# Kernel tuning notes

Hardware: AMD Instinct MI355X
Metric: run time of the kernel (lower is better)

Reference implementation:

```python
import jax, jax.numpy as jnp
import numpy as np

B, C, N, K, OUT = 4, 128, 8192, 20, 128


def setup_inputs() -> dict:
    key = jax.random.key(0)
    k1, k2, k3 = jax.random.split(key, 3)
    x = jax.random.normal(k1, (B, C, N), dtype=jnp.float32)
    W = jax.random.normal(k2, (OUT, 2 * C), dtype=jnp.float32) * 0.02  # 1x1 conv weight over 2C edge channels
    b = jnp.zeros((OUT,), dtype=jnp.float32)
    return {"x": x, "W": W, "b": b}


def _knn_idx(x, k):
    # x: [B, C, N]; pairwise_distance = -||xi - xj||^2 (larger = closer)
    inner = -2.0 * jnp.einsum('bcn,bcm->bnm', x, x)          # [B,N,N]
    xx = jnp.sum(x * x, axis=1)                               # [B,N]
    pd = -xx[:, :, None] - inner - xx[:, None, :]             # [B,N,N]
    return jax.lax.top_k(pd, k)[1]                            # [B,N,k] int32


def reference(x, W, b):
    k = K
    idx = _knn_idx(x, k)                                      # [B,N,k]
    xt = jnp.transpose(x, (0, 2, 1))                          # [B,N,C]
    nbr = jax.vmap(lambda xb, ib: xb[ib])(xt, idx)            # [B,N,k,C] gather
    center = jnp.broadcast_to(xt[:, :, None, :], nbr.shape)   # [B,N,k,C]
    # torch: cat((x, x - feature), dim=3)
    edge = jnp.concatenate([center, center - nbr], axis=-1)   # [B,N,k,2C]
    # 1x1 Conv2d over channel dim + ReLU
    h = jnp.einsum('bnkc,oc->bonk', edge, W) + b[None, :, None, None]
    h = jax.nn.relu(h)
    # aggregate over neighbors (EdgeConv max pooling)
    return jnp.max(h, axis=-1)                                # [B,OUT,N]
```

## Files before the change

### kernel.cpp

```cpp
#include <hip/hip_runtime.h>
#include <float.h>

#define Bz   4
#define Cz   128
#define Nz   8192
#define Kz   20
#define OUTz 128

__global__ __launch_bounds__(256) void xx_kernel(const float* __restrict__ x,
                                                 float* __restrict__ xx) {
    int t = blockIdx.x * 256 + threadIdx.x;
    int b = t >> 13;
    int n = t & (Nz - 1);
    const float* xp = x + (size_t)b * Cz * Nz + n;
    float s = 0.f;
#pragma unroll 8
    for (int c = 0; c < Cz; ++c) {
        float v = xp[(size_t)c * Nz];
        s = fmaf(v, v, s);
    }
    xx[t] = s;
}

__global__ __launch_bounds__(256) void knn_kernel(const float* __restrict__ x,
                                                  const float* __restrict__ xxg,
                                                  int* __restrict__ idxout) {
    const int b  = blockIdx.y;
    const int q0 = blockIdx.x * 64;

    __shared__ __align__(16) float Ald[128 * 64];
    __shared__ __align__(16) float buf2[2 * 8 * 256];
    float* bufA = buf2;
    float* bufB = buf2 + 2048;
    float* sc   = buf2;

    const int tid  = threadIdx.x;
    const int tx   = tid & 31;
    const int ty   = tid >> 5;
    const int lane = tid & 63;
    const int wid  = tid >> 6;

    const float* xb = x + (size_t)b * Cz * Nz;

    {
        int q4 = (tid & 15) * 4;
        int c0 = tid >> 4;
#pragma unroll
        for (int rep = 0; rep < 8; ++rep) {
            int c = c0 + rep * 16;
            *(float4*)&Ald[c * 64 + q4] =
                *(const float4*)&xb[(size_t)c * Nz + q0 + q4];
        }
    }

    float tv[Kz];
    int   ti[Kz];
#pragma unroll
    for (int s = 0; s < Kz; ++s) { tv[s] = -FLT_MAX; ti[s] = 0; }
    float wv = -FLT_MAX;
    int wslot = 0;
    const int orow = wid * 16 + lane;
    const int srow = wid * 16 + (lane & 15);
    const int part = lane >> 4;

    float4 st0[2], st1[2];

#define LOADCHUNK(dst, kj, ch)                                                \
    {                                                                         \
        _Pragma("unroll")                                                     \
        for (int i = 0; i < 2; ++i)                                           \
            dst[i] = *(const float4*)&xb[(size_t)((ch) * 8 + ty) * Nz + (kj) + tx * 4 + i * 128]; \
    }

#define WRITECHUNK(src, buf)                                                  \
    {                                                                         \
        _Pragma("unroll")                                                     \
        for (int i = 0; i < 2; ++i)                                           \
            *(float4*)&(buf)[ty * 256 + tx * 4 + i * 128] = src[i];           \
    }

#define COMPUTECHUNK(buf, ch)                                                 \
    {                                                                         \
        _Pragma("unroll")                                                     \
        for (int cc = 0; cc < 8; ++cc) {                                      \
            float4 a0 = *(const float4*)&Ald[((ch) * 8 + cc) * 64 + ty * 8];  \
            float4 a1 = *(const float4*)&Ald[((ch) * 8 + cc) * 64 + ty * 8 + 4]; \
            float4 b0 = *(const float4*)&(buf)[cc * 256 + tx * 4];            \
            float4 b1 = *(const float4*)&(buf)[cc * 256 + 128 + tx * 4];      \
            float av[8] = {a0.x, a0.y, a0.z, a0.w, a1.x, a1.y, a1.z, a1.w};   \
            float bv[8] = {b0.x, b0.y, b0.z, b0.w, b1.x, b1.y, b1.z, b1.w};   \
            _Pragma("unroll")                                                 \
            for (int q = 0; q < 8; ++q) {                                     \
                _Pragma("unroll")                                             \
                for (int k = 0; k < 8; ++k)                                   \
                    acc[q][k] = fmaf(av[q], bv[k], acc[q][k]);                \
            }                                                                 \
        }                                                                     \
    }

#define EXTRACT(pm_, gbase_)                                                  \
    {                                                                         \
        unsigned long long pm = (pm_);                                        \
        while (pm) {                                                          \
            int j = __ffsll(pm) - 1;                                          \
            pm &= pm - 1;                                                     \
            float s = sc[orow * 64 + ((j + 4 * orow) & 63)];                  \
            if (s > wv) {                                                     \
                int gj = (gbase_) + j;                                        \
                _Pragma("unroll")                                             \
                for (int s2 = 0; s2 < Kz; ++s2) {                             \
                    bool hit = (s2 == wslot);                                 \
                    tv[s2] = hit ? s : tv[s2];                                \
                    ti[s2] = hit ? gj : ti[s2];                               \
                }                                                             \
                wv = tv[0]; wslot = 0;                                        \
                _Pragma("unroll")                                             \
                for (int s2 = 1; s2 < Kz; ++s2)                               \
                    if (tv[s2] < wv) { wv = tv[s2]; wslot = s2; }             \
            }                                                                 \
        }                                                                     \
    }

    LOADCHUNK(st0, 0, 0);

#pragma unroll 1
    for (int kt = 0; kt < Nz / 256; ++kt) {
        const int kj0 = kt * 256;
        const int kjn = ((kt + 1) & (Nz / 256 - 1)) * 256;

        float acc[8][8];
#pragma unroll
        for (int q = 0; q < 8; ++q)
#pragma unroll
            for (int k = 0; k < 8; ++k) acc[q][k] = 0.f;

#pragma unroll 1
        for (int cp = 0; cp < 8; ++cp) {
            const int e = 2 * cp;
            WRITECHUNK(st0, bufA);
            __syncthreads();
            LOADCHUNK(st1, kj0, e + 1);
            COMPUTECHUNK(bufA, e);
            WRITECHUNK(st1, bufB);
            __syncthreads();
            if (e == 14) { LOADCHUNK(st0, kjn, 0); }
            else         { LOADCHUNK(st0, kj0, e + 2); }
            COMPUTECHUNK(bufB, e + 1);
        }
        __syncthreads();

        float4 xxlo = *(const float4*)&xxg[b * Nz + kj0 + tx * 4];
        float4 xxhi = *(const float4*)&xxg[b * Nz + kj0 + 128 + tx * 4];
        float xxa[8] = {xxlo.x, xxlo.y, xxlo.z, xxlo.w,
                        xxhi.x, xxhi.y, xxhi.z, xxhi.w};
        const int txh = tx >> 4;
        const int cl0 = (tx & 15) * 4;

#pragma unroll
        for (int h = 0; h < 4; ++h) {
            if (txh == (h & 1)) {
                const int qs = (h >> 1) * 4;
#pragma unroll
                for (int dq = 0; dq < 8; ++dq) {
                    int r = ty * 8 + dq;
                    float4 w;
                    w.x = 2.f * acc[dq][qs + 0] - xxa[qs + 0];
                    w.y = 2.f * acc[dq][qs + 1] - xxa[qs + 1];
                    w.z = 2.f * acc[dq][qs + 2] - xxa[qs + 2];
                    w.w = 2.f * acc[dq][qs + 3] - xxa[qs + 3];
                    *(float4*)&sc[r * 64 + ((cl0 + 4 * r) & 63)] = w;
                }
            }
            __syncthreads();

            float wvb = __shfl(wv, lane & 15);
            unsigned m = 0;
#pragma unroll
            for (int g = 0; g < 4; ++g) {
                int col = part * 16 + g * 4;
                float4 v = *(const float4*)&sc[srow * 64 + ((col + 4 * srow) & 63)];
                m |= (unsigned)(v.x > wvb) << (4 * g + 0);
                m |= (unsigned)(v.y > wvb) << (4 * g + 1);
                m |= (unsigned)(v.z > wvb) << (4 * g + 2);
                m |= (unsigned)(v.w > wvb) << (4 * g + 3);
            }
            unsigned long long f = (unsigned long long)m << (16 * part);
            f |= __shfl_xor(f, 16);
            f |= __shfl_xor(f, 32);
            if (lane < 16) { EXTRACT(f, kj0 + h * 64); }
            __syncthreads();
        }
    }

    if (lane < 16) {
        size_t base = ((size_t)b * Nz + q0 + orow) * Kz;
#pragma unroll
        for (int s = 0; s < Kz; ++s) idxout[base + s] = ti[s];
    }
#undef LOADCHUNK
#undef WRITECHUNK
#undef COMPUTECHUNK
#undef EXTRACT
}

__global__ __launch_bounds__(256) void feat_kernel(const float* __restrict__ x,
                                                   const float* __restrict__ W,
                                                   const float* __restrict__ bias,
                                                   float* __restrict__ Y) {
    const int gp0 = blockIdx.x * 64;
    const int b   = gp0 >> 13;
    const int n0  = gp0 & (Nz - 1);
    const int o0  = blockIdx.y * 64;

    __shared__ __align__(16) float xt[128 * 64];
    __shared__ __align__(16) float wt[128 * 64];

    const int tid = threadIdx.x;
    const int tx  = tid & 15;
    const int ty  = tid >> 4;

    {
        int li = tid & 63;
        int c0 = tid >> 6;
        const float* xbp = x + (size_t)b * Cz * Nz + n0;
#pragma unroll
        for (int rep = 0; rep < 32; ++rep) {
            int c = c0 + rep * 4;
            xt[c * 64 + li] = xbp[(size_t)c * Nz + li];
        }
    }
    {
        int lo = tid & 63;
        int c0 = tid >> 6;
        int oo = o0 + lo;
#pragma unroll
        for (int rep = 0; rep < 32; ++rep) {
            int c = c0 + rep * 4;
            float w;
            if (oo < 128) w = W[oo * 256 + c] + W[oo * 256 + 128 + c];
            else          w = W[(oo - 128) * 256 + 128 + c];
            wt[c * 64 + lo] = w;
        }
    }
    __syncthreads();

    float acc[4][4];
#pragma unroll
    for (int di = 0; di < 4; ++di)
#pragma unroll
        for (int dj = 0; dj < 4; ++dj) acc[di][dj] = 0.f;

    const int aoff = ty * 4;
    const int boff = tx * 4;
#pragma unroll 8
    for (int c = 0; c < 128; ++c) {
        float4 a  = *(const float4*)&xt[c * 64 + aoff];
        float4 ww = *(const float4*)&wt[c * 64 + boff];
        float av[4] = {a.x, a.y, a.z, a.w};
        float wvv[4] = {ww.x, ww.y, ww.z, ww.w};
#pragma unroll
        for (int di = 0; di < 4; ++di)
#pragma unroll
            for (int dj = 0; dj < 4; ++dj)
                acc[di][dj] = fmaf(av[di], wvv[dj], acc[di][dj]);
    }

    float4 bv = make_float4(0.f, 0.f, 0.f, 0.f);
    if (o0 < 128) bv = *(const float4*)&bias[o0 + tx * 4];
#pragma unroll
    for (int di = 0; di < 4; ++di) {
        float4 r;
        r.x = acc[di][0] + bv.x;
        r.y = acc[di][1] + bv.y;
        r.z = acc[di][2] + bv.z;
        r.w = acc[di][3] + bv.w;
        *(float4*)&Y[(size_t)(gp0 + ty * 4 + di) * 256 + o0 + tx * 4] = r;
    }
}

__global__ __launch_bounds__(256) void gather_kernel(const int* __restrict__ idxg,
                                                     const float* __restrict__ Y,
                                                     float* __restrict__ out) {
    const int gp0 = blockIdx.x * 64;
    const int b   = gp0 >> 13;
    const int n0  = gp0 & (Nz - 1);

    __shared__ int lidx[64 * 21];
    const int tid = threadIdx.x;
    for (int t = tid; t < 64 * Kz; t += 256) {
        int p = t / Kz, j = t - p * Kz;
        lidx[p * 21 + j] = idxg[(size_t)(gp0 + p) * Kz + j];
    }
    __syncthreads();

    const int p  = tid & 63;
    const int o0 = (tid >> 6) * 32;

    float mn[32];
#pragma unroll
    for (int q = 0; q < 32; ++q) mn[q] = FLT_MAX;

    for (int j = 0; j < Kz; ++j) {
        int m = lidx[p * 21 + j];
        const float4* vr =
            (const float4*)(Y + (size_t)(b * Nz + m) * 256 + 128 + o0);
#pragma unroll
        for (int q = 0; q < 8; ++q) {
            float4 v4 = vr[q];
            mn[4 * q + 0] = fminf(mn[4 * q + 0], v4.x);
            mn[4 * q + 1] = fminf(mn[4 * q + 1], v4.y);
            mn[4 * q + 2] = fminf(mn[4 * q + 2], v4.z);
            mn[4 * q + 3] = fminf(mn[4 * q + 3], v4.w);
        }
    }

    const float4* ur = (const float4*)(Y + (size_t)(gp0 + p) * 256 + o0);
#pragma unroll
    for (int q = 0; q < 8; ++q) {
        float4 u4 = ur[q];
        float r0 = fmaxf(u4.x - mn[4 * q + 0], 0.f);
        float r1 = fmaxf(u4.y - mn[4 * q + 1], 0.f);
        float r2 = fmaxf(u4.z - mn[4 * q + 2], 0.f);
        float r3 = fmaxf(u4.w - mn[4 * q + 3], 0.f);
        size_t ob = ((size_t)b * OUTz + o0 + 4 * q) * Nz + n0 + p;
        out[ob + 0 * Nz] = r0;
        out[ob + 1 * Nz] = r1;
        out[ob + 2 * Nz] = r2;
        out[ob + 3 * Nz] = r3;
    }
}

extern "C" void kernel_launch(void* const* d_in, const int* in_sizes, int n_in,
                              void* d_out, int out_size, void* d_ws, size_t ws_size,
                              hipStream_t stream) {
    const float* x    = (const float*)d_in[0];
    const float* W    = (const float*)d_in[1];
    const float* bias = (const float*)d_in[2];
    float* out = (float*)d_out;

    char* ws = (char*)d_ws;
    float* xx  = (float*)ws;
    int*   idx = (int*)(ws + (1 << 17));
    float* Y   = (float*)(ws + (4 << 20));

    xx_kernel<<<dim3(Bz * Nz / 256), dim3(256), 0, stream>>>(x, xx);

    knn_kernel<<<dim3(Nz / 64, Bz), dim3(256), 0, stream>>>(x, xx, idx);

    feat_kernel<<<dim3(Bz * Nz / 64, 4), dim3(256), 0, stream>>>(x, W, bias, Y);

    gather_kernel<<<dim3(Bz * Nz / 64), dim3(256), 0, stream>>>(idx, Y, out);
}
```

Baseline: 1.296 ms.

## Split KNN candidate range across two blocks and merge partial top-k lists

The KNN kernel now processes only half of the candidate points per block, using a third grid dimension, and writes partial top-k values and indices to workspace. A new merge kernel combines the two partial lists per query into the final indices. This doubles the number of blocks to improve GPU occupancy and load balance, at the cost of extra workspace traffic, a second kernel launch, and a fresh threshold per half that triggers more insertions.

```diff
diff --git a/kernel.cpp b/kernel.cpp
--- a/kernel.cpp
+++ b/kernel.cpp
@@ -24,9 +24,12 @@
 
 __global__ __launch_bounds__(256) void knn_kernel(const float* __restrict__ x,
                                                   const float* __restrict__ xxg,
-                                                  int* __restrict__ idxout) {
+                                                  float* __restrict__ pval,
+                                                  int* __restrict__ pidx) {
     const int b  = blockIdx.y;
     const int q0 = blockIdx.x * 64;
+    const int hz = blockIdx.z;
+    const int kb = hz * (Nz / 2);
 
     __shared__ __align__(16) float Ald[128 * 64];
     __shared__ __align__(16) float buf2[2 * 8 * 256];
@@ -121,12 +124,12 @@
         }                                                                     \
     }
 
-    LOADCHUNK(st0, 0, 0);
+    LOADCHUNK(st0, kb, 0);
 
 #pragma unroll 1
-    for (int kt = 0; kt < Nz / 256; ++kt) {
-        const int kj0 = kt * 256;
-        const int kjn = ((kt + 1) & (Nz / 256 - 1)) * 256;
+    for (int kt = 0; kt < Nz / 2 / 256; ++kt) {
+        const int kj0 = kb + kt * 256;
+        const int kjn = kb + (((kt + 1) & (Nz / 2 / 256 - 1)) * 256);
 
         float acc[8][8];
 #pragma unroll
@@ -193,14 +196,56 @@
     }
 
     if (lane < 16) {
-        size_t base = ((size_t)b * Nz + q0 + orow) * Kz;
-#pragma unroll
-        for (int s = 0; s < Kz; ++s) idxout[base + s] = ti[s];
+        size_t base = ((size_t)hz * Bz * Nz + (size_t)b * Nz + q0 + orow) * Kz;
+#pragma unroll
+        for (int s = 0; s < Kz; ++s) { pval[base + s] = tv[s]; pidx[base + s] = ti[s]; }
     }
 #undef LOADCHUNK
 #undef WRITECHUNK
 #undef COMPUTECHUNK
 #undef EXTRACT
+}
+
+__global__ __launch_bounds__(256) void merge_kernel(const float* __restrict__ pval,
+                                                    const int* __restrict__ pidx,
+                                                    int* __restrict__ idxout) {
+    const int r = blockIdx.x * 256 + threadIdx.x;
+    const float* v0 = pval + (size_t)r * Kz;
+    const float* v1 = pval + ((size_t)Bz * Nz + r) * Kz;
+    const int*   i0 = pidx + (size_t)r * Kz;
+    const int*   i1 = pidx + ((size_t)Bz * Nz + r) * Kz;
+
+    float tv[Kz]; int ti[Kz];
+#pragma unroll
+    for (int s = 0; s < Kz; ++s) { tv[s] = v0[s]; ti[s] = i0[s]; }
+    float wv = tv[0]; int wi = ti[0]; int wslot = 0;
+#pragma unroll
+    for (int s = 1; s < Kz; ++s) {
+        bool worse = (tv[s] < wv) || (tv[s] == wv && ti[s] > wi);
+        if (worse) { wv = tv[s]; wi = ti[s]; wslot = s; }
+    }
+#pragma unroll 1
+    for (int c = 0; c < Kz; ++c) {
+        float cv = v1[c]; int ci = i1[c];
+        bool better = (cv > wv) || (cv == wv && ci < wi);
+        if (better) {
+#pragma unroll
+            for (int s = 0; s < Kz; ++s) {
+                bool hit = (s == wslot);
+                tv[s] = hit ? cv : tv[s];
+                ti[s] = hit ? ci : ti[s];
+            }
+            wv = tv[0]; wi = ti[0]; wslot = 0;
+#pragma unroll
+            for (int s = 1; s < Kz; ++s) {
+                bool worse = (tv[s] < wv) || (tv[s] == wv && ti[s] > wi);
+                if (worse) { wv = tv[s]; wi = ti[s]; wslot = s; }
+            }
+        }
+    }
+    size_t base = (size_t)r * Kz;
+#pragma unroll
+    for (int s = 0; s < Kz; ++s) idxout[base + s] = ti[s];
 }
 
 __global__ __launch_bounds__(256) void feat_kernel(const float* __restrict__ x,
@@ -339,13 +384,17 @@
     float* out = (float*)d_out;
 
     char* ws = (char*)d_ws;
-    float* xx  = (float*)ws;
-    int*   idx = (int*)(ws + (1 << 17));
-    float* Y   = (float*)(ws + (4 << 20));
+    float* xx   = (float*)ws;
+    int*   idx  = (int*)(ws + (1 << 17));
+    float* pval = (float*)(ws + (4 << 20));
+    int*   pidx = (int*)(ws + (10 << 20));
+    float* Y    = (float*)(ws + (4 << 20));
 
     xx_kernel<<<dim3(Bz * Nz / 256), dim3(256), 0, stream>>>(x, xx);
 
-    knn_kernel<<<dim3(Nz / 64, Bz), dim3(256), 0, stream>>>(x, xx, idx);
+    knn_kernel<<<dim3(Nz / 64, Bz, 2), dim3(256), 0, stream>>>(x, xx, pval, pidx);
+
+    merge_kernel<<<dim3(Bz * Nz / 256), dim3(256), 0, stream>>>(pval, pidx, idx);
 
     feat_kernel<<<dim3(Bz * Nz / 64, 4), dim3(256), 0, stream>>>(x, W, bias, Y);
 
```

Result: slower. 1.412 ms (+8.9%).

## Stream kNN key tile from global memory into registers, drop LDS staging

Applied to the files above, without the earlier changes.

The kNN distance GEMM stops staging key columns through double-buffered shared memory with barriers. Each thread now loads its float4 of key columns straight from global memory into registers, prefetching four channels ahead, and reads the query tile from LDS as broadcast. The register tile changes from 8x8 to 16x4 per thread, which removes the per-chunk __syncthreads and LDS writes. In exchange, each key element is loaded by all four waves instead of once per block, which raises global/L2 traffic, and each FMA now needs more LDS reads.

```diff
diff --git a/kernel.cpp b/kernel.cpp
--- a/kernel.cpp
+++ b/kernel.cpp
@@ -29,14 +29,9 @@
     const int q0 = blockIdx.x * 64;
 
     __shared__ __align__(16) float Ald[128 * 64];
-    __shared__ __align__(16) float buf2[2 * 8 * 256];
-    float* bufA = buf2;
-    float* bufB = buf2 + 2048;
-    float* sc   = buf2;
+    __shared__ __align__(16) float sc[64 * 64];
 
     const int tid  = threadIdx.x;
-    const int tx   = tid & 31;
-    const int ty   = tid >> 5;
     const int lane = tid & 63;
     const int wid  = tid >> 6;
 
@@ -52,6 +47,7 @@
                 *(const float4*)&xb[(size_t)c * Nz + q0 + q4];
         }
     }
+    __syncthreads();
 
     float tv[Kz];
     int   ti[Kz];
@@ -62,39 +58,27 @@
     const int orow = wid * 16 + lane;
     const int srow = wid * 16 + (lane & 15);
     const int part = lane >> 4;
-
-    float4 st0[2], st1[2];
-
-#define LOADCHUNK(dst, kj, ch)                                                \
+    const int aoff = wid * 16;
+
+#define CSTEP(vb, cc)                                                         \
     {                                                                         \
+        const float4 cur_ = vb;                                               \
+        vb = *(const float4*)&bp[(size_t)(((cc) + 4) & 127) * Nz];            \
+        const float* ar_ = &Ald[(cc) * 64 + aoff];                            \
+        float4 a0_ = *(const float4*)(ar_);                                   \
+        float4 a1_ = *(const float4*)(ar_ + 4);                               \
+        float4 a2_ = *(const float4*)(ar_ + 8);                               \
+        float4 a3_ = *(const float4*)(ar_ + 12);                              \
+        float av_[16] = {a0_.x, a0_.y, a0_.z, a0_.w,                          \
+                         a1_.x, a1_.y, a1_.z, a1_.w,                          \
+                         a2_.x, a2_.y, a2_.z, a2_.w,                          \
+                         a3_.x, a3_.y, a3_.z, a3_.w};                         \
         _Pragma("unroll")                                                     \
-        for (int i = 0; i < 2; ++i)                                           \
-            dst[i] = *(const float4*)&xb[(size_t)((ch) * 8 + ty) * Nz + (kj) + tx * 4 + i * 128]; \
-    }
-
-#define WRITECHUNK(src, buf)                                                  \
-    {                                                                         \
-        _Pragma("unroll")                                                     \
-        for (int i = 0; i < 2; ++i)                                           \
-            *(float4*)&(buf)[ty * 256 + tx * 4 + i * 128] = src[i];           \
-    }
-
-#define COMPUTECHUNK(buf, ch)                                                 \
-    {                                                                         \
-        _Pragma("unroll")                                                     \
-        for (int cc = 0; cc < 8; ++cc) {                                      \
-            float4 a0 = *(const float4*)&Ald[((ch) * 8 + cc) * 64 + ty * 8];  \
-            float4 a1 = *(const float4*)&Ald[((ch) * 8 + cc) * 64 + ty * 8 + 4]; \
-            float4 b0 = *(const float4*)&(buf)[cc * 256 + tx * 4];            \
-            float4 b1 = *(const float4*)&(buf)[cc * 256 + 128 + tx * 4];      \
-            float av[8] = {a0.x, a0.y, a0.z, a0.w, a1.x, a1.y, a1.z, a1.w};   \
-            float bv[8] = {b0.x, b0.y, b0.z, b0.w, b1.x, b1.y, b1.z, b1.w};   \
-            _Pragma("unroll")                                                 \
-            for (int q = 0; q < 8; ++q) {                                     \
-                _Pragma("unroll")                                             \
-                for (int k = 0; k < 8; ++k)                                   \
-                    acc[q][k] = fmaf(av[q], bv[k], acc[q][k]);                \
-            }                                                                 \
+        for (int q = 0; q < 16; ++q) {                                        \
+            acc[q][0] = fmaf(av_[q], cur_.x, acc[q][0]);                      \
+            acc[q][1] = fmaf(av_[q], cur_.y, acc[q][1]);                      \
+            acc[q][2] = fmaf(av_[q], cur_.z, acc[q][2]);                      \
+            acc[q][3] = fmaf(av_[q], cur_.w, acc[q][3]);                      \
         }                                                                     \
     }
 
@@ -121,54 +105,48 @@
         }                                                                     \
     }
 
-    LOADCHUNK(st0, 0, 0);
-
 #pragma unroll 1
-    for (int kt = 0; kt < Nz / 256; ++kt) {
-        const int kj0 = kt * 256;
-        const int kjn = ((kt + 1) & (Nz / 256 - 1)) * 256;
-
-        float acc[8][8];
-#pragma unroll
-        for (int q = 0; q < 8; ++q)
-#pragma unroll
-            for (int k = 0; k < 8; ++k) acc[q][k] = 0.f;
+    for (int kp = 0; kp < Nz / 256; ++kp) {
+        const float* bp = xb + kp * 256 + 4 * lane;
+
+        float acc[16][4];
+#pragma unroll
+        for (int q = 0; q < 16; ++q)
+#pragma unroll
+            for (int i = 0; i < 4; ++i) acc[q][i] = 0.f;
+
+        float4 vb0 = *(const float4*)&bp[0];
+        float4 vb1 = *(const float4*)&bp[(size_t)1 * Nz];
+        float4 vb2 = *(const float4*)&bp[(size_t)2 * Nz];
+        float4 vb3 = *(const float4*)&bp[(size_t)3 * Nz];
 
 #pragma unroll 1
-        for (int cp = 0; cp < 8; ++cp) {
-            const int e = 2 * cp;
-            WRITECHUNK(st0, bufA);
-            __syncthreads();
-            LOADCHUNK(st1, kj0, e + 1);
-            COMPUTECHUNK(bufA, e);
-            WRITECHUNK(st1, bufB);
-            __syncthreads();
-            if (e == 14) { LOADCHUNK(st0, kjn, 0); }
-            else         { LOADCHUNK(st0, kj0, e + 2); }
-            COMPUTECHUNK(bufB, e + 1);
-        }
-        __syncthreads();
-
-        float4 xxlo = *(const float4*)&xxg[b * Nz + kj0 + tx * 4];
-        float4 xxhi = *(const float4*)&xxg[b * Nz + kj0 + 128 + tx * 4];
-        float xxa[8] = {xxlo.x, xxlo.y, xxlo.z, xxlo.w,
-                        xxhi.x, xxhi.y, xxhi.z, xxhi.w};
-        const int txh = tx >> 4;
-        const int cl0 = (tx & 15) * 4;
-
+        for (int c4 = 0; c4 < 16; ++c4) {
+            const int c = 8 * c4;
+            CSTEP(vb0, c + 0)
+            CSTEP(vb1, c + 1)
+            CSTEP(vb2, c + 2)
+            CSTEP(vb3, c + 3)
+            CSTEP(vb0, c + 4)
+            CSTEP(vb1, c + 5)
+            CSTEP(vb2, c + 6)
+            CSTEP(vb3, c + 7)
+        }
+
+        const float4 xxk = *(const float4*)&xxg[b * Nz + kp * 256 + 4 * lane];
 #pragma unroll
         for (int h = 0; h < 4; ++h) {
-            if (txh == (h & 1)) {
-                const int qs = (h >> 1) * 4;
-#pragma unroll
-                for (int dq = 0; dq < 8; ++dq) {
-                    int r = ty * 8 + dq;
+            if ((lane >> 4) == h) {
+                const int cl = (lane & 15) * 4;
+#pragma unroll
+                for (int dq = 0; dq < 16; ++dq) {
+                    int r = wid * 16 + dq;
                     float4 w;
-                    w.x = 2.f * acc[dq][qs + 0] - xxa[qs + 0];
-                    w.y = 2.f * acc[dq][qs + 1] - xxa[qs + 1];
-                    w.z = 2.f * acc[dq][qs + 2] - xxa[qs + 2];
-                    w.w = 2.f * acc[dq][qs + 3] - xxa[qs + 3];
-                    *(float4*)&sc[r * 64 + ((cl0 + 4 * r) & 63)] = w;
+                    w.x = 2.f * acc[dq][0] - xxk.x;
+                    w.y = 2.f * acc[dq][1] - xxk.y;
+                    w.z = 2.f * acc[dq][2] - xxk.z;
+                    w.w = 2.f * acc[dq][3] - xxk.w;
+                    *(float4*)&sc[r * 64 + ((cl + 4 * r) & 63)] = w;
                 }
             }
             __syncthreads();
@@ -187,7 +165,7 @@
             unsigned long long f = (unsigned long long)m << (16 * part);
             f |= __shfl_xor(f, 16);
             f |= __shfl_xor(f, 32);
-            if (lane < 16) { EXTRACT(f, kj0 + h * 64); }
+            if (lane < 16) { EXTRACT(f, kp * 256 + h * 64); }
             __syncthreads();
         }
     }
@@ -197,9 +175,7 @@
 #pragma unroll
         for (int s = 0; s < Kz; ++s) idxout[base + s] = ti[s];
     }
-#undef LOADCHUNK
-#undef WRITECHUNK
-#undef COMPUTECHUNK
+#undef CSTEP
 #undef EXTRACT
 }
 
```

Result: slower. 2.260 ms (+74.4%).

## Load key tiles directly from global into registers, dropping LDS staging

Applied to the files above, without the earlier changes.

The kNN distance GEMM no longer stages the 256-wide key tile through double-buffered shared memory with block-wide barriers. Each thread instead streams its own key columns from global memory into a 4-deep register prefetch ring and consumes them directly. The aim is to remove LDS writes and __syncthreads from the inner channel loop, and to shrink shared memory to a dedicated score buffer. In exchange, each wavefront row (the 8 ty groups) loads the same key data redundantly from global/L2, and prefetch depth is limited, so memory latency may be exposed.

```diff
diff --git a/kernel.cpp b/kernel.cpp
--- a/kernel.cpp
+++ b/kernel.cpp
@@ -29,10 +29,7 @@
     const int q0 = blockIdx.x * 64;
 
     __shared__ __align__(16) float Ald[128 * 64];
-    __shared__ __align__(16) float buf2[2 * 8 * 256];
-    float* bufA = buf2;
-    float* bufB = buf2 + 2048;
-    float* sc   = buf2;
+    __shared__ __align__(16) float sc[64 * 64];
 
     const int tid  = threadIdx.x;
     const int tx   = tid & 31;
@@ -52,6 +49,7 @@
                 *(const float4*)&xb[(size_t)c * Nz + q0 + q4];
         }
     }
+    __syncthreads();
 
     float tv[Kz];
     int   ti[Kz];
@@ -63,38 +61,28 @@
     const int srow = wid * 16 + (lane & 15);
     const int part = lane >> 4;
 
-    float4 st0[2], st1[2];
-
-#define LOADCHUNK(dst, kj, ch)                                                \
+#define CSTEP(u, cc)                                                          \
     {                                                                         \
+        const float4 cur0_ = rb0[u];                                          \
+        const float4 cur1_ = rb1[u];                                          \
+        const int cn_ = ((cc) + 4) & 127;                                     \
+        rb0[u] = *(const float4*)&bp0[(size_t)cn_ * Nz];                      \
+        rb1[u] = *(const float4*)&bp1[(size_t)cn_ * Nz];                      \
+        const float* ar_ = &Ald[(cc) * 64 + ty * 8];                          \
+        float4 a0_ = *(const float4*)(ar_);                                   \
+        float4 a1_ = *(const float4*)(ar_ + 4);                               \
+        float av_[8] = {a0_.x, a0_.y, a0_.z, a0_.w,                           \
+                        a1_.x, a1_.y, a1_.z, a1_.w};                          \
         _Pragma("unroll")                                                     \
-        for (int i = 0; i < 2; ++i)                                           \
-            dst[i] = *(const float4*)&xb[(size_t)((ch) * 8 + ty) * Nz + (kj) + tx * 4 + i * 128]; \
-    }
-
-#define WRITECHUNK(src, buf)                                                  \
-    {                                                                         \
-        _Pragma("unroll")                                                     \
-        for (int i = 0; i < 2; ++i)                                           \
-            *(float4*)&(buf)[ty * 256 + tx * 4 + i * 128] = src[i];           \
-    }
-
-#define COMPUTECHUNK(buf, ch)                                                 \
-    {                                                                         \
-        _Pragma("unroll")                                                     \
-        for (int cc = 0; cc < 8; ++cc) {                                      \
-            float4 a0 = *(const float4*)&Ald[((ch) * 8 + cc) * 64 + ty * 8];  \
-            float4 a1 = *(const float4*)&Ald[((ch) * 8 + cc) * 64 + ty * 8 + 4]; \
-            float4 b0 = *(const float4*)&(buf)[cc * 256 + tx * 4];            \
-            float4 b1 = *(const float4*)&(buf)[cc * 256 + 128 + tx * 4];      \
-            float av[8] = {a0.x, a0.y, a0.z, a0.w, a1.x, a1.y, a1.z, a1.w};   \
-            float bv[8] = {b0.x, b0.y, b0.z, b0.w, b1.x, b1.y, b1.z, b1.w};   \
-            _Pragma("unroll")                                                 \
-            for (int q = 0; q < 8; ++q) {                                     \
-                _Pragma("unroll")                                             \
-                for (int k = 0; k < 8; ++k)                                   \
-                    acc[q][k] = fmaf(av[q], bv[k], acc[q][k]);                \
-            }                                                                 \
+        for (int q = 0; q < 8; ++q) {                                         \
+            acc[q][0] = fmaf(av_[q], cur0_.x, acc[q][0]);                     \
+            acc[q][1] = fmaf(av_[q], cur0_.y, acc[q][1]);                     \
+            acc[q][2] = fmaf(av_[q], cur0_.z, acc[q][2]);                     \
+            acc[q][3] = fmaf(av_[q], cur0_.w, acc[q][3]);                     \
+            acc[q][4] = fmaf(av_[q], cur1_.x, acc[q][4]);                     \
+            acc[q][5] = fmaf(av_[q], cur1_.y, acc[q][5]);                     \
+            acc[q][6] = fmaf(av_[q], cur1_.z, acc[q][6]);                     \
+            acc[q][7] = fmaf(av_[q], cur1_.w, acc[q][7]);                     \
         }                                                                     \
     }
 
@@ -121,12 +109,11 @@
         }                                                                     \
     }
 
-    LOADCHUNK(st0, 0, 0);
-
 #pragma unroll 1
     for (int kt = 0; kt < Nz / 256; ++kt) {
         const int kj0 = kt * 256;
-        const int kjn = ((kt + 1) & (Nz / 256 - 1)) * 256;
+        const float* bp0 = xb + kj0 + tx * 4;
+        const float* bp1 = xb + kj0 + 128 + tx * 4;
 
         float acc[8][8];
 #pragma unroll
@@ -134,20 +121,21 @@
 #pragma unroll
             for (int k = 0; k < 8; ++k) acc[q][k] = 0.f;
 
+        float4 rb0[4], rb1[4];
+#pragma unroll
+        for (int i = 0; i < 4; ++i) {
+            rb0[i] = *(const float4*)&bp0[(size_t)i * Nz];
+            rb1[i] = *(const float4*)&bp1[(size_t)i * Nz];
+        }
+
 #pragma unroll 1
-        for (int cp = 0; cp < 8; ++cp) {
-            const int e = 2 * cp;
-            WRITECHUNK(st0, bufA);
-            __syncthreads();
-            LOADCHUNK(st1, kj0, e + 1);
-            COMPUTECHUNK(bufA, e);
-            WRITECHUNK(st1, bufB);
-            __syncthreads();
-            if (e == 14) { LOADCHUNK(st0, kjn, 0); }
-            else         { LOADCHUNK(st0, kj0, e + 2); }
-            COMPUTECHUNK(bufB, e + 1);
-        }
-        __syncthreads();
+        for (int c4 = 0; c4 < 32; ++c4) {
+            const int c = 4 * c4;
+            CSTEP(0, c + 0)
+            CSTEP(1, c + 1)
+            CSTEP(2, c + 2)
+            CSTEP(3, c + 3)
+        }
 
         float4 xxlo = *(const float4*)&xxg[b * Nz + kj0 + tx * 4];
         float4 xxhi = *(const float4*)&xxg[b * Nz + kj0 + 128 + tx * 4];
@@ -197,9 +185,7 @@
 #pragma unroll
         for (int s = 0; s < Kz; ++s) idxout[base + s] = ti[s];
     }
-#undef LOADCHUNK
-#undef WRITECHUNK
-#undef COMPUTECHUNK
+#undef CSTEP
 #undef EXTRACT
 }
 
```

Result: slower. 3.479 ms (+168.4%).
